# Performance work log

Measured on AMD Instinct MI355X. Metric: run time of the kernel, lower is better.

Reference implementation:

```python
import jax, jax.numpy as jnp
import numpy as np

B, L, H, D, M = 4, 2048, 16, 64, 128
EPS = 1e-6


def _create_projection_matrix(key, m, d):
    nb_full_blocks = m // d
    keys = jax.random.split(key, nb_full_blocks + 2)
    blocks = []
    for i in range(nb_full_blocks):
        unstructured = jax.random.normal(keys[i], (d, d), dtype=jnp.float32)
        q, _ = jnp.linalg.qr(unstructured)
        blocks.append(q.T)
    remaining = m - nb_full_blocks * d
    if remaining > 0:
        unstructured = jax.random.normal(keys[nb_full_blocks], (d, d), dtype=jnp.float32)
        q, _ = jnp.linalg.qr(unstructured)
        blocks.append(q.T[:remaining])
    final = jnp.concatenate(blocks, axis=0)  # [m, d]
    multiplier = jnp.linalg.norm(jax.random.normal(keys[-1], (m, d), dtype=jnp.float32), axis=1)
    return multiplier[:, None] * final


def setup_inputs() -> dict:
    key = jax.random.key(0)
    kq, kk, kv, kp = jax.random.split(key, 4)
    return {
        "q": jax.random.normal(kq, (B, L, H, D), dtype=jnp.float32),
        "k": jax.random.normal(kk, (B, L, H, D), dtype=jnp.float32),
        "v": jax.random.normal(kv, (B, L, H, D), dtype=jnp.float32),
        "projection_matrix": _create_projection_matrix(kp, M, D),
    }


def _softmax_kernel(data, proj, is_query, eps=EPS):
    # data: [B,L,H,D], proj: [M,D]
    data = (data.shape[-1] ** -0.25) * data
    ratio = proj.shape[0] ** -0.5
    data_dash = jnp.einsum('blhd,md->blhm', data, proj)  # [B,L,H,M]
    diag = jnp.sum(data * data, axis=-1, keepdims=True) * 0.5  # [B,L,H,1]
    if is_query:
        mx = jnp.max(data_dash, axis=-1, keepdims=True)
    else:
        mx = jnp.max(data_dash, axis=(1, 3), keepdims=True)
    return ratio * (jnp.exp(data_dash - diag - mx) + eps)


def reference(q, k, v, projection_matrix):
    qp = _softmax_kernel(q, projection_matrix, True)   # [B,L,H,M]
    kp = _softmax_kernel(k, projection_matrix, False)  # [B,L,H,M]
    # move L to the front for the causal scan
    qs = jnp.swapaxes(qp, 0, 1)  # [L,B,H,M]
    ks = jnp.swapaxes(kp, 0, 1)  # [L,B,H,M]
    vs = jnp.swapaxes(v, 0, 1)   # [L,B,H,D]

    def step(carry, inp):
        s, dsum = carry                 # s: [B,H,M,D], dsum: [B,H,M]
        q_t, k_t, v_t = inp
        s = s + k_t[..., :, None] * v_t[..., None, :]  # outer product accumulate
        dsum = dsum + k_t
        num = jnp.einsum('bhmd,bhm->bhd', s, q_t)      # [B,H,D]
        den = jnp.einsum('bhm,bhm->bh', q_t, dsum)     # [B,H]
        return (s, dsum), (num, den)

    init = (jnp.zeros((qs.shape[1], qs.shape[2], qs.shape[3], vs.shape[3]), qs.dtype),
            jnp.zeros_like(ks[0]))
    _, (nums, dens) = jax.lax.scan(step, init, (qs, ks, vs))
    av = jnp.swapaxes(nums, 0, 1)          # [B,L,H,D]
    norm = jnp.swapaxes(dens, 0, 1)[..., None]  # [B,L,H,1]
    return av / norm
```

## Files before the change

### kernel.cpp

```cpp
#include <hip/hip_runtime.h>
#include <math.h>

#define B_ 4
#define L_ 2048
#define H_ 16
#define D_ 64
#define M_ 128
#define TC_ 64
#define NC_ (L_ / TC_)
#define EPSK 1e-6f
#define DATA_SCALE 0.35355339059327379f
#define RATIO 0.08838834764831845f

typedef __bf16 bf16;
typedef bf16 bf16x4 __attribute__((ext_vector_type(4)));
typedef bf16 bf16x8 __attribute__((ext_vector_type(8)));
typedef float floatx4 __attribute__((ext_vector_type(4)));

#define PK64 72
#define FS_ 136

__device__ __forceinline__ unsigned pk(bf16 a, bf16 b) {
    return (unsigned)__builtin_bit_cast(unsigned short, a) |
           ((unsigned)__builtin_bit_cast(unsigned short, b) << 16);
}

__device__ __forceinline__ unsigned enc_f(float f) {
    unsigned u = __float_as_uint(f);
    return (u & 0x80000000u) ? ~u : (u | 0x80000000u);
}
__device__ __forceinline__ float dec_f(unsigned u) {
    unsigned b = (u & 0x80000000u) ? (u ^ 0x80000000u) : ~u;
    return __uint_as_float(b);
}

__global__ __launch_bounds__(256) void proj_split(const float* __restrict__ proj,
                                                  bf16* __restrict__ pfh,
                                                  bf16* __restrict__ pfl,
                                                  unsigned* __restrict__ mx) {
    int f = blockIdx.x * 256 + threadIdx.x;
    if (blockIdx.x == 0 && threadIdx.x < B_ * H_) mx[threadIdx.x] = 0u;
    int tc = f >> 7, k0h = (f >> 6) & 1, lane = f & 63;
    int lr = lane & 15, quad = lane >> 4;
    const float* src = proj + (16 * tc + lr) * 64 + k0h * 32 + quad * 8;
    float4 x0 = *(const float4*)src;
    float4 x1 = *(const float4*)(src + 4);
    float a[8] = {x0.x, x0.y, x0.z, x0.w, x1.x, x1.y, x1.z, x1.w};
    bf16x8 hi, lo;
#pragma unroll
    for (int e = 0; e < 8; e++) {
        bf16 h = (bf16)a[e];
        hi[e] = h;
        lo[e] = (bf16)(a[e] - (float)h);
    }
    *(bf16x8*)(pfh + (size_t)f * 8) = hi;
    *(bf16x8*)(pfl + (size_t)f * 8) = lo;
}

__global__ __launch_bounds__(256) void feat_max(const float* __restrict__ k,
                                                const bf16* __restrict__ pfh,
                                                unsigned* __restrict__ mxk) {
    __shared__ float wred[4];
    int tid = threadIdx.x;
    int blk = blockIdx.x;
    int c = blk & 31, h = (blk >> 5) & 15, b = blk >> 9;
    int l0 = c * 64;
    int w = tid >> 6, lane = tid & 63, lr = lane & 15, quad = lane >> 4;

    const float* drow = k +
        ((size_t)(b * L_ + l0 + 16 * w + lr) * H_ + h) * D_ + quad * 8;
    bf16x8 ah[2];
#pragma unroll
    for (int k0 = 0; k0 < 2; k0++) {
        float4 x0 = *(const float4*)(drow + k0 * 32);
        float4 x1 = *(const float4*)(drow + k0 * 32 + 4);
        float a[8] = {x0.x, x0.y, x0.z, x0.w, x1.x, x1.y, x1.z, x1.w};
#pragma unroll
        for (int e = 0; e < 8; e++) ah[k0][e] = (bf16)(DATA_SCALE * a[e]);
    }

    floatx4 acc[8];
#pragma unroll
    for (int tc = 0; tc < 8; tc++) acc[tc] = (floatx4){0.f, 0.f, 0.f, 0.f};
    const bf16x8* ph = (const bf16x8*)pfh + lane;
#pragma unroll
    for (int tc = 0; tc < 8; tc++)
#pragma unroll
        for (int k0 = 0; k0 < 2; k0++) {
            bf16x8 bh = ph[(tc * 2 + k0) * 64];
            acc[tc] = __builtin_amdgcn_mfma_f32_16x16x32_bf16(ah[k0], bh, acc[tc], 0, 0, 0);
        }

    float mm = acc[0][0];
#pragma unroll
    for (int tc = 0; tc < 8; tc++)
#pragma unroll
        for (int reg = 0; reg < 4; reg++) mm = fmaxf(mm, acc[tc][reg]);
#pragma unroll
    for (int off = 1; off < 64; off <<= 1) mm = fmaxf(mm, __shfl_xor(mm, off, 64));
    if (lane == 0) wred[w] = mm;
    __syncthreads();
    if (tid == 0) {
        float g = fmaxf(fmaxf(wred[0], wred[1]), fmaxf(wred[2], wred[3]));
        atomicMax(&mxk[b * H_ + h], enc_f(g));
    }
}

__global__ __launch_bounds__(256) void feat_k(const float* __restrict__ kin,
                                              const bf16* __restrict__ pfh,
                                              const bf16* __restrict__ pfl,
                                              const unsigned* __restrict__ mxk,
                                              bf16* __restrict__ kp) {
    __shared__ __align__(16) bf16 sc[64 * 130];
    int tid = threadIdx.x;
    int blk = blockIdx.x;
    int c = blk & 31, h = (blk >> 5) & 15, b = blk >> 9;
    int l0 = c * 64;
    int w = tid >> 6, lane = tid & 63, lr = lane & 15, quad = lane >> 4;

    const float* drow = kin +
        ((size_t)(b * L_ + l0 + 16 * w + lr) * H_ + h) * D_ + quad * 8;
    bf16x8 ah[2], al[2];
    float ss = 0.f;
#pragma unroll
    for (int k0 = 0; k0 < 2; k0++) {
        float4 x0 = *(const float4*)(drow + k0 * 32);
        float4 x1 = *(const float4*)(drow + k0 * 32 + 4);
        float a[8] = {x0.x, x0.y, x0.z, x0.w, x1.x, x1.y, x1.z, x1.w};
#pragma unroll
        for (int e = 0; e < 8; e++) {
            float s = DATA_SCALE * a[e];
            ss += s * s;
            bf16 hh = (bf16)s;
            ah[k0][e] = hh;
            al[k0][e] = (bf16)(s - (float)hh);
        }
    }
    ss += __shfl_xor(ss, 16, 64);
    ss += __shfl_xor(ss, 32, 64);
    float ssrow = 0.5f * ss;

    floatx4 acc[8];
#pragma unroll
    for (int tc = 0; tc < 8; tc++) acc[tc] = (floatx4){0.f, 0.f, 0.f, 0.f};
    const bf16x8* ph = (const bf16x8*)pfh + lane;
    const bf16x8* pl = (const bf16x8*)pfl + lane;
#pragma unroll
    for (int tc = 0; tc < 8; tc++)
#pragma unroll
        for (int k0 = 0; k0 < 2; k0++) {
            bf16x8 bh = ph[(tc * 2 + k0) * 64];
            bf16x8 bl = pl[(tc * 2 + k0) * 64];
            acc[tc] = __builtin_amdgcn_mfma_f32_16x16x32_bf16(ah[k0], bh, acc[tc], 0, 0, 0);
            acc[tc] = __builtin_amdgcn_mfma_f32_16x16x32_bf16(al[k0], bh, acc[tc], 0, 0, 0);
            acc[tc] = __builtin_amdgcn_mfma_f32_16x16x32_bf16(ah[k0], bl, acc[tc], 0, 0, 0);
        }

    int t0 = 16 * w + 4 * quad;
    float mxg = dec_f(mxk[b * H_ + h]);
#pragma unroll
    for (int reg = 0; reg < 4; reg++) {
        float dg = __shfl(ssrow, 4 * quad + reg, 64);
        float sh = dg + mxg;
#pragma unroll
        for (int tc = 0; tc < 8; tc++) {
            float val = RATIO * (__expf(acc[tc][reg] - sh) + EPSK);
            sc[(t0 + reg) * 130 + 16 * tc + lr] = (bf16)val;
        }
    }
    __syncthreads();

    bf16* kout = kp + (size_t)blk * 8192;
#pragma unroll
    for (int i = 0; i < 16; i++) {
        int e = tid + 256 * i;
        int row = e >> 6, mp = e & 63;
        *(unsigned*)(kout + row * 128 + 2 * mp) =
            pk(sc[row * 130 + 2 * mp], sc[row * 130 + 2 * mp + 1]);
    }
}

__global__ __launch_bounds__(256) void chunk_v(const bf16* __restrict__ kp,
                                               const float* __restrict__ v,
                                               bf16* __restrict__ S,
                                               float* __restrict__ ds,
                                               bf16* __restrict__ vbT) {
    __shared__ __align__(16) bf16 kT[128 * PK64];
    __shared__ __align__(16) bf16 vT[64 * PK64];
    int tid = threadIdx.x;
    int blk = blockIdx.x;
    int c = blk & 31, bh = blk >> 5;
    int h = bh & 15, b = bh >> 4;
    int l0 = c * 64;
    int w = tid >> 6, lane = tid & 63, lr = lane & 15, quad = lane >> 4;

    const bf16* kpt = kp + (size_t)blk * 8192;
#pragma unroll
    for (int i = 0; i < 4; i++) {
        int m8 = w * 4 + i;
        bf16x8 kv = *(const bf16x8*)(kpt + lane * 128 + m8 * 8);
#pragma unroll
        for (int e = 0; e < 8; e++) kT[(m8 * 8 + e) * PK64 + lane] = kv[e];
    }
    {
        const float* vrow = v + ((size_t)(b * L_ + l0 + lane) * H_ + h) * D_;
#pragma unroll
        for (int i = 0; i < 4; i++) {
            int d4 = w * 4 + i;
            float4 x = *(const float4*)(vrow + d4 * 4);
            vT[(d4 * 4 + 0) * PK64 + lane] = (bf16)x.x;
            vT[(d4 * 4 + 1) * PK64 + lane] = (bf16)x.y;
            vT[(d4 * 4 + 2) * PK64 + lane] = (bf16)x.z;
            vT[(d4 * 4 + 3) * PK64 + lane] = (bf16)x.w;
        }
    }
    __syncthreads();

    floatx4 acc[8];
#pragma unroll
    for (int tc = 0; tc < 8; tc++) acc[tc] = (floatx4){0.f, 0.f, 0.f, 0.f};
#pragma unroll
    for (int k0 = 0; k0 < 64; k0 += 32) {
        bf16x8 a = *(const bf16x8*)(vT + (16 * w + lr) * PK64 + k0 + quad * 8);
#pragma unroll
        for (int tc = 0; tc < 8; tc++) {
            bf16x8 bb = *(const bf16x8*)(kT + (16 * tc + lr) * PK64 + k0 + quad * 8);
            acc[tc] = __builtin_amdgcn_mfma_f32_16x16x32_bf16(a, bb, acc[tc], 0, 0, 0);
        }
    }

    {
        size_t ob = (size_t)(bh * D_) * (size_t)L_ + l0;
#pragma unroll
        for (int i = 0; i < 8; i++) {
            int e2 = tid + 256 * i;
            int d = e2 >> 5, tau2 = (e2 & 31) * 2;
            *(unsigned*)(vbT + ob + (size_t)d * L_ + tau2) =
                *(const unsigned*)(vT + d * PK64 + tau2);
        }
    }

    float dsv = 0.f;
    {
        int m = tid >> 1, half = tid & 1;
        const bf16x8* kr = (const bf16x8*)(kT + m * PK64 + half * 32);
#pragma unroll
        for (int j = 0; j < 4; j++) {
            bf16x8 vv = kr[j];
#pragma unroll
            for (int e = 0; e < 8; e++) dsv += (float)vv[e];
        }
        dsv += __shfl_xor(dsv, 1, 64);
    }
    __syncthreads();

    bf16* scr = kT;
    int d0 = 16 * w + 4 * quad;
#pragma unroll
    for (int tc = 0; tc < 8; tc++)
#pragma unroll
        for (int reg = 0; reg < 4; reg++)
            scr[(d0 + reg) * 128 + 16 * tc + lr] = (bf16)acc[tc][reg];
    if ((tid & 1) == 0) ds[(size_t)blk * M_ + (tid >> 1)] = dsv;
    __syncthreads();
#pragma unroll
    for (int i = 0; i < 4; i++) {
        int e = tid + 256 * i;
        ((uint4*)S)[(size_t)blk * 1024 + e] = ((const uint4*)scr)[e];
    }
}

__global__ void prefix_SD(unsigned* __restrict__ S, float* __restrict__ ds) {
    int blk = blockIdx.x;
    int seg = blk & 15, bh = blk >> 4;
    int p = seg * 256 + threadIdx.x;
    size_t base = (size_t)bh * NC_ * 4096 + p;
    unsigned uv[NC_];
#pragma unroll
    for (int c = 0; c < NC_; c++) uv[c] = S[base + (size_t)c * 4096];
    float c0 = 0.f, c1 = 0.f;
#pragma unroll
    for (int c = 0; c < NC_; c++) {
        unsigned u = uv[c];
        float f0 = (float)__builtin_bit_cast(bf16, (unsigned short)(u & 0xffffu));
        float f1 = (float)__builtin_bit_cast(bf16, (unsigned short)(u >> 16));
        S[base + (size_t)c * 4096] = pk((bf16)c0, (bf16)c1);
        c0 += f0; c1 += f1;
    }
    if (seg == 0 && threadIdx.x < 128) {
        int m = threadIdx.x;
        size_t dbase = (size_t)bh * NC_ * M_ + m;
        float dv[NC_];
#pragma unroll
        for (int c = 0; c < NC_; c++) dv[c] = ds[dbase + (size_t)c * M_];
        float carry = 0.f;
#pragma unroll
        for (int c = 0; c < NC_; c++) {
            ds[dbase + (size_t)c * M_] = carry;
            carry += dv[c];
        }
    }
}

__global__ __launch_bounds__(256, 4) void attn_q(const float* __restrict__ q,
                                                 const bf16* __restrict__ pfh,
                                                 const bf16* __restrict__ pfl,
                                                 const bf16* __restrict__ kp,
                                                 const bf16* __restrict__ vbT,
                                                 const bf16* __restrict__ Sp,
                                                 const float* __restrict__ dp,
                                                 float* __restrict__ out) {
    __shared__ __align__(16) bf16 fsc[64 * FS_];
    __shared__ __align__(16) bf16 vT[64 * PK64];
    __shared__ float dprevL[128];
    bf16* sc = fsc;

    int tid = threadIdx.x;
    int blk = blockIdx.x;
    int c = blk & 31, bh = blk >> 5;
    int h = bh & 15, b = bh >> 4;
    int l0 = c * 64;
    int w = tid >> 6, lane = tid & 63, lr = lane & 15, quad = lane >> 4;

#pragma unroll
    for (int i = 0; i < 2; i++) {
        int ch = tid + 256 * i;
        int d = ch >> 3, c8 = ch & 7;
        *(uint4*)(vT + d * PK64 + c8 * 8) =
            ((const uint4*)vbT)[(((size_t)bh * D_ + d) * L_ + l0) / 8 + c8];
    }
    if (tid < 128) dprevL[tid] = dp[(size_t)blk * M_ + tid];

    const float* drow = q +
        ((size_t)(b * L_ + l0 + 16 * w + lr) * H_ + h) * D_ + quad * 8;
    bf16x8 ah[2], al[2];
    float ss = 0.f;
#pragma unroll
    for (int k0 = 0; k0 < 2; k0++) {
        float4 x0 = *(const float4*)(drow + k0 * 32);
        float4 x1 = *(const float4*)(drow + k0 * 32 + 4);
        float a[8] = {x0.x, x0.y, x0.z, x0.w, x1.x, x1.y, x1.z, x1.w};
#pragma unroll
        for (int e = 0; e < 8; e++) {
            float s = DATA_SCALE * a[e];
            ss += s * s;
            bf16 hh = (bf16)s;
            ah[k0][e] = hh;
            al[k0][e] = (bf16)(s - (float)hh);
        }
    }
    ss += __shfl_xor(ss, 16, 64);
    ss += __shfl_xor(ss, 32, 64);
    float ssrow = 0.5f * ss;

    floatx4 facc[8];
#pragma unroll
    for (int tc = 0; tc < 8; tc++) facc[tc] = (floatx4){0.f, 0.f, 0.f, 0.f};
    {
        const bf16x8* ph = (const bf16x8*)pfh + lane;
        const bf16x8* pl = (const bf16x8*)pfl + lane;
#pragma unroll
        for (int tc = 0; tc < 8; tc++)
#pragma unroll
            for (int k0 = 0; k0 < 2; k0++) {
                bf16x8 bh = ph[(tc * 2 + k0) * 64];
                bf16x8 bl = pl[(tc * 2 + k0) * 64];
                facc[tc] = __builtin_amdgcn_mfma_f32_16x16x32_bf16(ah[k0], bh, facc[tc], 0, 0, 0);
                facc[tc] = __builtin_amdgcn_mfma_f32_16x16x32_bf16(al[k0], bh, facc[tc], 0, 0, 0);
                facc[tc] = __builtin_amdgcn_mfma_f32_16x16x32_bf16(ah[k0], bl, facc[tc], 0, 0, 0);
            }
    }
    int t0 = 16 * w + 4 * quad;
#pragma unroll
    for (int reg = 0; reg < 4; reg++) {
        float m = facc[0][reg];
#pragma unroll
        for (int tc = 1; tc < 8; tc++) m = fmaxf(m, facc[tc][reg]);
        m = fmaxf(m, __shfl_xor(m, 1, 64));
        m = fmaxf(m, __shfl_xor(m, 2, 64));
        m = fmaxf(m, __shfl_xor(m, 4, 64));
        m = fmaxf(m, __shfl_xor(m, 8, 64));
        float dg = __shfl(ssrow, 4 * quad + reg, 64);
        float sh = dg + m;
#pragma unroll
        for (int tc = 0; tc < 8; tc++) {
            float val = RATIO * (__expf(facc[tc][reg] - sh) + EPSK);
            fsc[(t0 + reg) * FS_ + 16 * tc + lr] = (bf16)val;
        }
    }
    __syncthreads();

    bf16x8 af[4];
#pragma unroll
    for (int k = 0; k < 4; k++)
        af[k] = *(const bf16x8*)(fsc + (16 * w + lr) * FS_ + 32 * k + quad * 8);

    float den0v = 0.f;
#pragma unroll
    for (int k = 0; k < 4; k++)
#pragma unroll
        for (int e = 0; e < 8; e++)
            den0v += (float)af[k][e] * dprevL[quad * 8 + 32 * k + e];
    den0v += __shfl_xor(den0v, 16, 64);
    den0v += __shfl_xor(den0v, 32, 64);

    floatx4 acc[4];
#pragma unroll
    for (int tc = 0; tc < 4; tc++) acc[tc] = (floatx4){0.f, 0.f, 0.f, 0.f};

    {
        const bf16* spb = Sp + (size_t)blk * 8192;
#pragma unroll
        for (int ki = 0; ki < 4; ki++) {
#pragma unroll
            for (int tc = 0; tc < 4; tc++) {
                bf16x8 bb = *(const bf16x8*)(spb + (16 * tc + lr) * 128 + 32 * ki + quad * 8);
                acc[tc] = __builtin_amdgcn_mfma_f32_16x16x32_bf16(af[ki], bb, acc[tc], 0, 0, 0);
            }
        }
    }

    floatx4 acc2[4];
#pragma unroll
    for (int tc = 0; tc < 4; tc++) acc2[tc] = (floatx4){0.f, 0.f, 0.f, 0.f};
    {
        const bf16* kpb = kp + (size_t)blk * 8192 + quad * 8;
#pragma unroll
        for (int ki = 0; ki < 4; ki++) {
            for (int tc = 0; tc <= w; tc++) {
                bf16x8 bb = *(const bf16x8*)(kpb + (16 * tc + lr) * 128 + 32 * ki);
                acc2[tc] = __builtin_amdgcn_mfma_f32_16x16x32_bf16(af[ki], bb, acc2[tc], 0, 0, 0);
            }
        }
    }
    __syncthreads();

    float densc[4];
    {
        float dsum[4] = {0.f, 0.f, 0.f, 0.f};
#pragma unroll
        for (int tc = 0; tc < 4; tc++) {
#pragma unroll
            for (int reg = 0; reg < 4; reg++) {
                int tg = t0 + reg, tau = 16 * tc + lr;
                float vv = (tc <= w) ? acc2[tc][reg] : 0.f;
                if (tau > tg) vv = 0.f;
                dsum[reg] += vv;
                sc[tg * PK64 + tau] = (bf16)vv;
            }
        }
#pragma unroll
        for (int reg = 0; reg < 4; reg++) {
            float s = dsum[reg];
            s += __shfl_xor(s, 1, 64);
            s += __shfl_xor(s, 2, 64);
            s += __shfl_xor(s, 4, 64);
            s += __shfl_xor(s, 8, 64);
            densc[reg] = s;
        }
    }

    {
        int kmax = (w >= 2) ? 64 : 32;
        for (int k0 = 0; k0 < kmax; k0 += 32) {
            bf16x8 a = *(const bf16x8*)(sc + (16 * w + lr) * PK64 + k0 + quad * 8);
#pragma unroll
            for (int tc = 0; tc < 4; tc++) {
                bf16x8 bb = *(const bf16x8*)(vT + (16 * tc + lr) * PK64 + k0 + quad * 8);
                acc[tc] = __builtin_amdgcn_mfma_f32_16x16x32_bf16(a, bb, acc[tc], 0, 0, 0);
            }
        }
    }

    {
        float inv[4];
#pragma unroll
        for (int reg = 0; reg < 4; reg++) {
            float d0 = __shfl(den0v, 4 * quad + reg, 64);
            inv[reg] = 1.0f / (d0 + densc[reg]);
        }
#pragma unroll
        for (int tc = 0; tc < 4; tc++)
#pragma unroll
            for (int reg = 0; reg < 4; reg++)
                out[((size_t)(b * L_ + l0 + t0 + reg) * H_ + h) * D_ + 16 * tc + lr] =
                    acc[tc][reg] * inv[reg];
    }
}

extern "C" void kernel_launch(void* const* d_in, const int* in_sizes, int n_in,
                              void* d_out, int out_size, void* d_ws, size_t ws_size,
                              hipStream_t stream) {
    const float* q = (const float*)d_in[0];
    const float* k = (const float*)d_in[1];
    const float* v = (const float*)d_in[2];
    const float* proj = (const float*)d_in[3];
    float* out = (float*)d_out;
    char* W = (char*)d_ws;

    bf16* kp   = (bf16*)(W);
    bf16* vbT  = (bf16*)(W + 33554432ull);
    bf16* S    = (bf16*)(W + 50331648ull);
    float* ds  = (float*)(W + 83886080ull);
    unsigned* mx = (unsigned*)(W + 84934656ull);
    bf16* pfh  = (bf16*)(W + 84934912ull);
    bf16* pfl  = (bf16*)(W + 84951296ull);

    hipLaunchKernelGGL(proj_split, dim3(4), dim3(256), 0, stream, proj, pfh, pfl, mx);
    hipLaunchKernelGGL(feat_max, dim3(2048), dim3(256), 0, stream, k, pfh, mx);
    hipLaunchKernelGGL(feat_k, dim3(2048), dim3(256), 0, stream, k, pfh, pfl, mx, kp);
    hipLaunchKernelGGL(chunk_v, dim3(2048), dim3(256), 0, stream, kp, v, S, ds, vbT);
    hipLaunchKernelGGL(prefix_SD, dim3(1024), dim3(256), 0, stream, (unsigned*)S, ds);
    hipLaunchKernelGGL(attn_q, dim3(2048), dim3(256), 0, stream,
                       q, pfh, pfl, kp, vbT, S, ds, out);
}
```

Measured before the change: 236.5 us.

## Store kp and S in MFMA fragment order and prefetch S fragments into registers

The producer kernels now write the kp feature map and the per-chunk state S in a layout that matches the MFMA B-operand fragments, so attn_q can fetch each fragment with one coalesced 16-byte load per lane. attn_q prefetches all 16 S fragments into registers at kernel entry, overlapping that load with the q projection. It also drops one __syncthreads by writing the causal score tile into fsc in place and deferring the den0 dot product until after the remaining barrier. The extra register use lowers launch_bounds occupancy from 4 to 3 blocks per CU.

```diff
diff --git a/kernel.cpp b/kernel.cpp
--- a/kernel.cpp
+++ b/kernel.cpp
@@ -170,13 +170,15 @@
     }
     __syncthreads();
 
-    bf16* kout = kp + (size_t)blk * 8192;
+    unsigned* kout = (unsigned*)(kp + (size_t)blk * 8192);
 #pragma unroll
     for (int i = 0; i < 16; i++) {
-        int e = tid + 256 * i;
-        int row = e >> 6, mp = e & 63;
-        *(unsigned*)(kout + row * 128 + 2 * mp) =
-            pk(sc[row * 130 + 2 * mp], sc[row * 130 + 2 * mp + 1]);
+        int u = tid + 256 * i;
+        int f = u >> 2, e0 = (u & 3) * 2;
+        int fi = f >> 6, fl = f & 63;
+        int tau = 16 * (fi & 3) + (fl & 15);
+        int m = 32 * (fi >> 2) + 8 * (fl >> 4) + e0;
+        kout[u] = pk(sc[tau * 130 + m], sc[tau * 130 + m + 1]);
     }
 }
 
@@ -198,7 +200,8 @@
 #pragma unroll
     for (int i = 0; i < 4; i++) {
         int m8 = w * 4 + i;
-        bf16x8 kv = *(const bf16x8*)(kpt + lane * 128 + m8 * 8);
+        bf16x8 kv = *(const bf16x8*)(kpt +
+            (((m8 >> 2) * 4 + (lane >> 4)) * 64 + (m8 & 3) * 16 + (lane & 15)) * 8);
 #pragma unroll
         for (int e = 0; e < 8; e++) kT[(m8 * 8 + e) * PK64 + lane] = kv[e];
     }
@@ -255,12 +258,13 @@
     __syncthreads();
 
     bf16* scr = kT;
-    int d0 = 16 * w + 4 * quad;
 #pragma unroll
     for (int tc = 0; tc < 8; tc++)
 #pragma unroll
         for (int reg = 0; reg < 4; reg++)
-            scr[(d0 + reg) * 128 + 16 * tc + lr] = (bf16)acc[tc][reg];
+            scr[((tc >> 1) * 4 + w) * 512 +
+                (((((tc & 1) << 1) | (lr >> 3)) * 16) + 4 * quad + reg) * 8 +
+                (lr & 7)] = (bf16)acc[tc][reg];
     if ((tid & 1) == 0) ds[(size_t)blk * M_ + (tid >> 1)] = dsv;
     __syncthreads();
 #pragma unroll
@@ -302,7 +306,7 @@
     }
 }
 
-__global__ __launch_bounds__(256, 4) void attn_q(const float* __restrict__ q,
+__global__ __launch_bounds__(256, 3) void attn_q(const float* __restrict__ q,
                                                  const bf16* __restrict__ pfh,
                                                  const bf16* __restrict__ pfl,
                                                  const bf16* __restrict__ kp,
@@ -313,7 +317,6 @@
     __shared__ __align__(16) bf16 fsc[64 * FS_];
     __shared__ __align__(16) bf16 vT[64 * PK64];
     __shared__ float dprevL[128];
-    bf16* sc = fsc;
 
     int tid = threadIdx.x;
     int blk = blockIdx.x;
@@ -322,6 +325,12 @@
     int l0 = c * 64;
     int w = tid >> 6, lane = tid & 63, lr = lane & 15, quad = lane >> 4;
 
+    bf16x8 spf[16];
+    {
+        const bf16x8* spb = (const bf16x8*)(Sp + (size_t)blk * 8192) + lane;
+#pragma unroll
+        for (int f = 0; f < 16; f++) spf[f] = spb[f * 64];
+    }
 #pragma unroll
     for (int i = 0; i < 2; i++) {
         int ch = tid + 256 * i;
@@ -388,52 +397,38 @@
             fsc[(t0 + reg) * FS_ + 16 * tc + lr] = (bf16)val;
         }
     }
-    __syncthreads();
 
     bf16x8 af[4];
 #pragma unroll
     for (int k = 0; k < 4; k++)
         af[k] = *(const bf16x8*)(fsc + (16 * w + lr) * FS_ + 32 * k + quad * 8);
 
-    float den0v = 0.f;
-#pragma unroll
-    for (int k = 0; k < 4; k++)
-#pragma unroll
-        for (int e = 0; e < 8; e++)
-            den0v += (float)af[k][e] * dprevL[quad * 8 + 32 * k + e];
-    den0v += __shfl_xor(den0v, 16, 64);
-    den0v += __shfl_xor(den0v, 32, 64);
-
     floatx4 acc[4];
 #pragma unroll
     for (int tc = 0; tc < 4; tc++) acc[tc] = (floatx4){0.f, 0.f, 0.f, 0.f};
 
-    {
-        const bf16* spb = Sp + (size_t)blk * 8192;
-#pragma unroll
-        for (int ki = 0; ki < 4; ki++) {
-#pragma unroll
-            for (int tc = 0; tc < 4; tc++) {
-                bf16x8 bb = *(const bf16x8*)(spb + (16 * tc + lr) * 128 + 32 * ki + quad * 8);
-                acc[tc] = __builtin_amdgcn_mfma_f32_16x16x32_bf16(af[ki], bb, acc[tc], 0, 0, 0);
-            }
-        }
-    }
+#pragma unroll
+    for (int ki = 0; ki < 4; ki++)
+#pragma unroll
+        for (int tc = 0; tc < 4; tc++)
+            acc[tc] = __builtin_amdgcn_mfma_f32_16x16x32_bf16(af[ki], spf[ki * 4 + tc],
+                                                              acc[tc], 0, 0, 0);
 
     floatx4 acc2[4];
 #pragma unroll
     for (int tc = 0; tc < 4; tc++) acc2[tc] = (floatx4){0.f, 0.f, 0.f, 0.f};
     {
-        const bf16* kpb = kp + (size_t)blk * 8192 + quad * 8;
-#pragma unroll
-        for (int ki = 0; ki < 4; ki++) {
-            for (int tc = 0; tc <= w; tc++) {
-                bf16x8 bb = *(const bf16x8*)(kpb + (16 * tc + lr) * 128 + 32 * ki);
-                acc2[tc] = __builtin_amdgcn_mfma_f32_16x16x32_bf16(af[ki], bb, acc2[tc], 0, 0, 0);
-            }
-        }
-    }
-    __syncthreads();
+        const bf16x8* kpb = (const bf16x8*)(kp + (size_t)blk * 8192) + lane;
+        bf16x8 kb[16];
+#pragma unroll
+        for (int ki = 0; ki < 4; ki++)
+            for (int tc = 0; tc <= w; tc++) kb[ki * 4 + tc] = kpb[(ki * 4 + tc) * 64];
+#pragma unroll
+        for (int ki = 0; ki < 4; ki++)
+            for (int tc = 0; tc <= w; tc++)
+                acc2[tc] = __builtin_amdgcn_mfma_f32_16x16x32_bf16(af[ki], kb[ki * 4 + tc],
+                                                                   acc2[tc], 0, 0, 0);
+    }
 
     float densc[4];
     {
@@ -446,7 +441,7 @@
                 float vv = (tc <= w) ? acc2[tc][reg] : 0.f;
                 if (tau > tg) vv = 0.f;
                 dsum[reg] += vv;
-                sc[tg * PK64 + tau] = (bf16)vv;
+                fsc[tg * FS_ + tau] = (bf16)vv;
             }
         }
 #pragma unroll
@@ -460,10 +455,21 @@
         }
     }
 
+    __syncthreads();
+
+    float den0v = 0.f;
+#pragma unroll
+    for (int k = 0; k < 4; k++)
+#pragma unroll
+        for (int e = 0; e < 8; e++)
+            den0v += (float)af[k][e] * dprevL[quad * 8 + 32 * k + e];
+    den0v += __shfl_xor(den0v, 16, 64);
+    den0v += __shfl_xor(den0v, 32, 64);
+
     {
         int kmax = (w >= 2) ? 64 : 32;
         for (int k0 = 0; k0 < kmax; k0 += 32) {
-            bf16x8 a = *(const bf16x8*)(sc + (16 * w + lr) * PK64 + k0 + quad * 8);
+            bf16x8 a = *(const bf16x8*)(fsc + (16 * w + lr) * FS_ + k0 + quad * 8);
 #pragma unroll
             for (int tc = 0; tc < 4; tc++) {
                 bf16x8 bb = *(const bf16x8*)(vT + (16 * tc + lr) * PK64 + k0 + quad * 8);
```

After: 267.5 us. 13.1% more time.
